# Performance work log

Measured on AMD Instinct MI355X. Metric: run time of the kernel, lower is better.

Reference implementation:

```python
import jax, jax.numpy as jnp
import numpy as np

N_NODES = 50000
N_GRAPHS = 128


def gcn_conv(x, edge_index, W, b, n_nodes):
    # PyG GCNConv: h = D^{-1/2}(A+I)D^{-1/2} (x W) + b
    h = x @ W  # [N, H]
    loop = jnp.arange(n_nodes)
    src = jnp.concatenate([edge_index[0], loop])
    dst = jnp.concatenate([edge_index[1], loop])
    deg = jax.ops.segment_sum(jnp.ones_like(dst, h.dtype), dst, num_segments=n_nodes)
    dinv = jnp.where(deg > 0, deg ** -0.5, 0.0)
    norm = dinv[src] * dinv[dst]  # [E+N]
    msgs = h[src] * norm[:, None]  # gather + normalize
    out = jax.ops.segment_sum(msgs, dst, num_segments=n_nodes)  # scatter-add
    return out + b


def setup_inputs() -> dict:
    key = jax.random.key(0)
    ks = jax.random.split(key, 8)
    F_in, H, L = 128, 128, 7
    x = jax.random.normal(ks[0], (N_NODES, F_in), dtype=jnp.float32)
    edge_index = jax.random.randint(ks[1], (2, 800000), 0, N_NODES, dtype=jnp.int64)
    batch = jnp.sort(jax.random.randint(ks[2], (N_NODES,), 0, N_GRAPHS, dtype=jnp.int64))
    s = lambda f: (1.0 / np.sqrt(f)).astype(np.float32)
    W1 = jax.random.normal(ks[3], (F_in, H), dtype=jnp.float32) * s(F_in)
    b1 = jnp.zeros((H,), jnp.float32)
    W2 = jax.random.normal(ks[4], (H, H), dtype=jnp.float32) * s(H)
    b2 = jnp.zeros((H,), jnp.float32)
    Wfc = jax.random.normal(ks[5], (H, L), dtype=jnp.float32) * s(H)
    bfc = jnp.zeros((L,), jnp.float32)
    return {"x": x, "edge_index": edge_index, "batch": batch,
            "W1": W1, "b1": b1, "W2": W2, "b2": b2, "Wfc": Wfc, "bfc": bfc}


def reference(x, edge_index, batch, W1, b1, W2, b2, Wfc, bfc):
    n = x.shape[0]
    h = jax.nn.relu(gcn_conv(x, edge_index, W1, b1, n))
    h = jax.nn.relu(gcn_conv(h, edge_index, W2, b2, n))
    # global_mean_pool over batch vector
    sums = jax.ops.segment_sum(h, batch, num_segments=N_GRAPHS)  # [G, H]
    cnt = jax.ops.segment_sum(jnp.ones((n,), h.dtype), batch, num_segments=N_GRAPHS)
    pooled = sums / jnp.maximum(cnt, 1.0)[:, None]
    return pooled @ Wfc + bfc  # [G, label_dim]
```

## Files before the change

kernel.cpp:

```cpp
#include <hip/hip_runtime.h>
#include <hip/hip_bf16.h>

#define HD 128
#define NL 7
#define BCAP 6144

typedef __attribute__((ext_vector_type(8))) short bf16x8;
typedef __attribute__((ext_vector_type(4))) float f32x4;

__device__ __forceinline__ unsigned short f2bf(float f) {
    __hip_bfloat16 b = __float2bfloat16(f);
    return *reinterpret_cast<unsigned short*>(&b);
}
__device__ __forceinline__ float bf2f(unsigned short u) {
    unsigned int x = ((unsigned int)u) << 16;
    return __uint_as_float(x);
}


__global__ __launch_bounds__(256) void k_prep(int* __restrict__ gbcur, int nb,
                                              float* __restrict__ sums, int m,
                                              const float* __restrict__ W1,
                                              const float* __restrict__ W2,
                                              unsigned short* __restrict__ Wt1,
                                              unsigned short* __restrict__ Wt2) {
    int i = blockIdx.x * 256 + threadIdx.x;
    if (i < nb) gbcur[i] = 0;
    if (i < m) sums[i] = 0.f;
    if (i < HD * HD) {
        int k = i >> 7, nn = i & 127;
        Wt1[nn * HD + k] = f2bf(W1[i]);
        Wt2[nn * HD + k] = f2bf(W2[i]);
    }
}


__global__ __launch_bounds__(256) void k_bucket(const int* __restrict__ src,
                                                const int* __restrict__ dst, int E,
                                                int* __restrict__ gbcur,
                                                int* __restrict__ stage, int nb) {
    __shared__ int lh[256];
    __shared__ int gb[256];
    int t = threadIdx.x;
    if (t < nb) lh[t] = 0;
    __syncthreads();

    int e0 = blockIdx.x * 4096;
    int bk[16]; int lr[16]; int rec[16];
    #pragma unroll
    for (int j = 0; j < 16; ++j) {
        int e = e0 + j * 256 + t;
        if (e < E) {
            int d = dst[e];
            int s = src[e];
            bk[j]  = d >> 8;
            rec[j] = ((d & 255) << 16) | s;
            lr[j]  = atomicAdd(&lh[bk[j]], 1);
        } else {
            bk[j] = -1; lr[j] = 0; rec[j] = 0;
        }
    }
    __syncthreads();
    if (t < nb) gb[t] = atomicAdd(&gbcur[t], lh[t]);
    __syncthreads();
    #pragma unroll
    for (int j = 0; j < 16; ++j) {
        if (bk[j] >= 0) {
            int p = gb[bk[j]] + lr[j];
            if (p < BCAP) stage[bk[j] * BCAP + p] = rec[j];
        }
    }
}


__global__ __launch_bounds__(256) void k_build_gemm1(
        const int* __restrict__ stage, const int* __restrict__ gbcnt,
        int* __restrict__ col, int* __restrict__ row_start,
        float* __restrict__ dinv,
        const float* __restrict__ X, const unsigned short* __restrict__ Wt,
        unsigned short* __restrict__ Y, int n, int nb) {
    __shared__ int rec_s[BCAP];
    __shared__ unsigned short rank_s[BCAP];
    __shared__ int hist[256];
    __shared__ int scan_s[256];
    __shared__ int base_s;
    int t = threadIdx.x;

    if ((int)blockIdx.x < nb) {
        int b = blockIdx.x;

        int cval = (t < nb) ? gbcnt[t] : 0;
        scan_s[t] = cval;
        __syncthreads();
        #pragma unroll
        for (int off = 1; off < 256; off <<= 1) {
            int v = (t >= off) ? scan_s[t - off] : 0;
            __syncthreads();
            scan_s[t] += v;
            __syncthreads();
        }
        if (t == b) base_s = scan_s[t] - cval;
        if (b == 0 && t == 0) row_start[n] = scan_s[nb - 1];
        __syncthreads();
        int base = base_s;
        int cnt  = min(gbcnt[b], BCAP);
        int node0 = b << 8;

        hist[t] = 0;
        __syncthreads();
        for (int e = t; e < cnt; e += 256) {
            int r = stage[b * BCAP + e];
            rec_s[e] = r;
            rank_s[e] = (unsigned short)atomicAdd(&hist[r >> 16], 1);
        }
        __syncthreads();

        int deg = hist[t];
        int node = node0 + t;
        if (node < n) dinv[node] = 1.0f / sqrtf((float)(deg + 1));

        scan_s[t] = deg;
        __syncthreads();
        #pragma unroll
        for (int off = 1; off < 256; off <<= 1) {
            int v = (t >= off) ? scan_s[t - off] : 0;
            __syncthreads();
            scan_s[t] += v;
            __syncthreads();
        }
        int lrs = scan_s[t] - deg;
        hist[t] = lrs;
        if (node < n) row_start[node] = base + lrs;
        __syncthreads();

        for (int e = t; e < cnt; e += 256) {
            int r = rec_s[e];
            col[base + hist[r >> 16] + rank_s[e]] = r & 0xFFFF;
        }
    } else {
        int wave = t >> 6, lane = t & 63;
        int lm = lane & 15, g = lane >> 4;
        int m0 = ((int)blockIdx.x - nb) * 64 + wave * 16;
        int row = m0 + lm;
        bool rok = row < n;

        f32x4 acc[8] = {};

        #pragma unroll
        for (int kb = 0; kb < 4; ++kb) {
            int k0 = kb * 32 + g * 8;
            bf16x8 a = {0, 0, 0, 0, 0, 0, 0, 0};
            if (rok) {
                const float* xp = X + (size_t)row * HD + k0;
                float4 v0 = *(const float4*)xp;
                float4 v1 = *(const float4*)(xp + 4);
                a[0] = (short)f2bf(v0.x); a[1] = (short)f2bf(v0.y);
                a[2] = (short)f2bf(v0.z); a[3] = (short)f2bf(v0.w);
                a[4] = (short)f2bf(v1.x); a[5] = (short)f2bf(v1.y);
                a[6] = (short)f2bf(v1.z); a[7] = (short)f2bf(v1.w);
            }
            #pragma unroll
            for (int nt = 0; nt < 8; ++nt) {
                int ncol = nt * 16 + lm;
                bf16x8 bfrag = *(const bf16x8*)(Wt + (size_t)ncol * HD + k0);
                acc[nt] = __builtin_amdgcn_mfma_f32_16x16x32_bf16(a, bfrag, acc[nt], 0, 0, 0);
            }
        }

        #pragma unroll
        for (int nt = 0; nt < 8; ++nt) {
            #pragma unroll
            for (int r = 0; r < 4; ++r) {
                int orow = m0 + g * 4 + r;
                if (orow < n) Y[(size_t)orow * HD + nt * 16 + lm] = f2bf(acc[nt][r]);
            }
        }
    }
}


__global__ __launch_bounds__(256) void k_gemm_mfma_bf(const unsigned short* __restrict__ X,
                                                      const unsigned short* __restrict__ Wt,
                                                      unsigned short* __restrict__ Y, int n) {
    int wave = threadIdx.x >> 6, lane = threadIdx.x & 63;
    int lm = lane & 15, g = lane >> 4;
    int m0 = blockIdx.x * 64 + wave * 16;
    int row = m0 + lm;
    bool rok = row < n;

    f32x4 acc[8] = {};

    #pragma unroll
    for (int kb = 0; kb < 4; ++kb) {
        int k0 = kb * 32 + g * 8;
        bf16x8 a = {0, 0, 0, 0, 0, 0, 0, 0};
        if (rok) a = *(const bf16x8*)(X + (size_t)row * HD + k0);
        #pragma unroll
        for (int nt = 0; nt < 8; ++nt) {
            int ncol = nt * 16 + lm;
            bf16x8 bfrag = *(const bf16x8*)(Wt + (size_t)ncol * HD + k0);
            acc[nt] = __builtin_amdgcn_mfma_f32_16x16x32_bf16(a, bfrag, acc[nt], 0, 0, 0);
        }
    }

    #pragma unroll
    for (int nt = 0; nt < 8; ++nt) {
        #pragma unroll
        for (int r = 0; r < 4; ++r) {
            int orow = m0 + g * 4 + r;
            if (orow < n) Y[(size_t)orow * HD + nt * 16 + lm] = f2bf(acc[nt][r]);
        }
    }
}


__global__ __launch_bounds__(256) void k_agg(const unsigned short* __restrict__ hin,
                                             const float* __restrict__ dinv,
                                             const int* __restrict__ row_start,
                                             const int* __restrict__ col,
                                             const float* __restrict__ bias,
                                             unsigned short* __restrict__ hout, int n) {
    int wave = threadIdx.x >> 6;
    int lane = threadIdx.x & 63;
    int v = blockIdx.x * 4 + wave;
    if (v >= n) return;

    int h  = lane >> 5;
    int li = lane & 31;
    int f  = li * 4;

    float dv = dinv[v];
    float a0 = 0.f, a1 = 0.f, a2 = 0.f, a3 = 0.f;

    int e  = row_start[v];
    int e1 = row_start[v + 1];

    for (; e + 8 <= e1; e += 8) {
        int s0 = col[e + h];
        int s1 = col[e + h + 2];
        int s2 = col[e + h + 4];
        int s3 = col[e + h + 6];
        float w0 = dinv[s0] * dv, w1 = dinv[s1] * dv;
        float w2 = dinv[s2] * dv, w3 = dinv[s3] * dv;
        ushort4 r0 = *(const ushort4*)(hin + (size_t)s0 * HD + f);
        ushort4 r1 = *(const ushort4*)(hin + (size_t)s1 * HD + f);
        ushort4 r2 = *(const ushort4*)(hin + (size_t)s2 * HD + f);
        ushort4 r3 = *(const ushort4*)(hin + (size_t)s3 * HD + f);
        a0 = fmaf(bf2f(r0.x), w0, a0); a1 = fmaf(bf2f(r0.y), w0, a1);
        a2 = fmaf(bf2f(r0.z), w0, a2); a3 = fmaf(bf2f(r0.w), w0, a3);
        a0 = fmaf(bf2f(r1.x), w1, a0); a1 = fmaf(bf2f(r1.y), w1, a1);
        a2 = fmaf(bf2f(r1.z), w1, a2); a3 = fmaf(bf2f(r1.w), w1, a3);
        a0 = fmaf(bf2f(r2.x), w2, a0); a1 = fmaf(bf2f(r2.y), w2, a1);
        a2 = fmaf(bf2f(r2.z), w2, a2); a3 = fmaf(bf2f(r2.w), w2, a3);
        a0 = fmaf(bf2f(r3.x), w3, a0); a1 = fmaf(bf2f(r3.y), w3, a1);
        a2 = fmaf(bf2f(r3.z), w3, a2); a3 = fmaf(bf2f(r3.w), w3, a3);
    }

    {
        #pragma unroll
        for (int j = 0; j < 4; ++j) {
            int idx = e + h + 2 * j;
            if (idx < e1) {
                int s = col[idx];
                float w = dinv[s] * dv;
                ushort4 r = *(const ushort4*)(hin + (size_t)s * HD + f);
                a0 = fmaf(bf2f(r.x), w, a0); a1 = fmaf(bf2f(r.y), w, a1);
                a2 = fmaf(bf2f(r.z), w, a2); a3 = fmaf(bf2f(r.w), w, a3);
            }
        }
    }

    a0 += __shfl_xor(a0, 32);
    a1 += __shfl_xor(a1, 32);
    a2 += __shfl_xor(a2, 32);
    a3 += __shfl_xor(a3, 32);

    if (h == 0) {
        ushort4 sv = *(const ushort4*)(hin + (size_t)v * HD + f);
        float selfw = dv * dv;
        float4 b = *(const float4*)(bias + f);
        ushort4 o;
        o.x = f2bf(fmaxf(fmaf(bf2f(sv.x), selfw, a0) + b.x, 0.f));
        o.y = f2bf(fmaxf(fmaf(bf2f(sv.y), selfw, a1) + b.y, 0.f));
        o.z = f2bf(fmaxf(fmaf(bf2f(sv.z), selfw, a2) + b.z, 0.f));
        o.w = f2bf(fmaxf(fmaf(bf2f(sv.w), selfw, a3) + b.w, 0.f));
        __builtin_nontemporal_store(*(unsigned long long*)&o,
            (unsigned long long*)(hout + (size_t)v * HD + f));
    }
}


__global__ __launch_bounds__(256) void k_agg_pool(const unsigned short* __restrict__ hin,
                                                  const float* __restrict__ dinv,
                                                  const int* __restrict__ row_start,
                                                  const int* __restrict__ col,
                                                  const float* __restrict__ bias,
                                                  const int* __restrict__ batch,
                                                  float* __restrict__ sums, int n) {
    __shared__ float lsum[4][HD];
    __shared__ int used[4];
    __shared__ int gbase_s;
    int t = threadIdx.x;

    if (t < 4) used[t] = 0;
    for (int i = t; i < 4 * HD; i += 256) ((float*)lsum)[i] = 0.f;
    int blk0 = blockIdx.x * 32;
    if (t == 0) gbase_s = batch[min(blk0, n - 1)];
    __syncthreads();
    int gbase = gbase_s;

    int wave = t >> 6;
    int lane = t & 63;
    int h  = lane >> 5;
    int li = lane & 31;
    int f  = li * 4;

    int v0 = blk0 + wave * 8;
    int vend = min(v0 + 8, n);

    float4 b = *(const float4*)(bias + f);
    float p0 = 0.f, p1 = 0.f, p2 = 0.f, p3 = 0.f;
    int curg = (v0 < n) ? batch[v0] : -1;

    for (int v = v0; v < vend; ++v) {
        float dv = dinv[v];
        float a0 = 0.f, a1 = 0.f, a2 = 0.f, a3 = 0.f;

        int e  = row_start[v];
        int e1 = row_start[v + 1];

        for (; e + 8 <= e1; e += 8) {
            int s0 = col[e + h];
            int s1 = col[e + h + 2];
            int s2 = col[e + h + 4];
            int s3 = col[e + h + 6];
            float w0 = dinv[s0] * dv, w1 = dinv[s1] * dv;
            float w2 = dinv[s2] * dv, w3 = dinv[s3] * dv;
            ushort4 r0 = *(const ushort4*)(hin + (size_t)s0 * HD + f);
            ushort4 r1 = *(const ushort4*)(hin + (size_t)s1 * HD + f);
            ushort4 r2 = *(const ushort4*)(hin + (size_t)s2 * HD + f);
            ushort4 r3 = *(const ushort4*)(hin + (size_t)s3 * HD + f);
            a0 = fmaf(bf2f(r0.x), w0, a0); a1 = fmaf(bf2f(r0.y), w0, a1);
            a2 = fmaf(bf2f(r0.z), w0, a2); a3 = fmaf(bf2f(r0.w), w0, a3);
            a0 = fmaf(bf2f(r1.x), w1, a0); a1 = fmaf(bf2f(r1.y), w1, a1);
            a2 = fmaf(bf2f(r1.z), w1, a2); a3 = fmaf(bf2f(r1.w), w1, a3);
            a0 = fmaf(bf2f(r2.x), w2, a0); a1 = fmaf(bf2f(r2.y), w2, a1);
            a2 = fmaf(bf2f(r2.z), w2, a2); a3 = fmaf(bf2f(r2.w), w2, a3);
            a0 = fmaf(bf2f(r3.x), w3, a0); a1 = fmaf(bf2f(r3.y), w3, a1);
            a2 = fmaf(bf2f(r3.z), w3, a2); a3 = fmaf(bf2f(r3.w), w3, a3);
        }

        #pragma unroll
        for (int j = 0; j < 4; ++j) {
            int idx = e + h + 2 * j;
            if (idx < e1) {
                int s = col[idx];
                float w = dinv[s] * dv;
                ushort4 r = *(const ushort4*)(hin + (size_t)s * HD + f);
                a0 = fmaf(bf2f(r.x), w, a0); a1 = fmaf(bf2f(r.y), w, a1);
                a2 = fmaf(bf2f(r.z), w, a2); a3 = fmaf(bf2f(r.w), w, a3);
            }
        }

        a0 += __shfl_xor(a0, 32);
        a1 += __shfl_xor(a1, 32);
        a2 += __shfl_xor(a2, 32);
        a3 += __shfl_xor(a3, 32);

        if (h == 0) {
            ushort4 sv = *(const ushort4*)(hin + (size_t)v * HD + f);
            float selfw = dv * dv;
            float ox = fmaxf(fmaf(bf2f(sv.x), selfw, a0) + b.x, 0.f);
            float oy = fmaxf(fmaf(bf2f(sv.y), selfw, a1) + b.y, 0.f);
            float oz = fmaxf(fmaf(bf2f(sv.z), selfw, a2) + b.z, 0.f);
            float ow = fmaxf(fmaf(bf2f(sv.w), selfw, a3) + b.w, 0.f);
            int g = batch[v];
            if (g != curg) {
                int slot = curg - gbase;
                if (slot >= 0 && slot < 4) {
                    atomicAdd(&lsum[slot][f],     p0);
                    atomicAdd(&lsum[slot][f + 1], p1);
                    atomicAdd(&lsum[slot][f + 2], p2);
                    atomicAdd(&lsum[slot][f + 3], p3);
                    used[slot] = 1;
                } else {
                    float* sp = sums + (size_t)curg * HD + f;
                    atomicAdd(sp,     p0);
                    atomicAdd(sp + 1, p1);
                    atomicAdd(sp + 2, p2);
                    atomicAdd(sp + 3, p3);
                }
                p0 = p1 = p2 = p3 = 0.f;
                curg = g;
            }
            p0 += ox; p1 += oy; p2 += oz; p3 += ow;
        }
    }

    if (h == 0 && curg >= 0) {
        int slot = curg - gbase;
        if (slot >= 0 && slot < 4) {
            atomicAdd(&lsum[slot][f],     p0);
            atomicAdd(&lsum[slot][f + 1], p1);
            atomicAdd(&lsum[slot][f + 2], p2);
            atomicAdd(&lsum[slot][f + 3], p3);
            used[slot] = 1;
        } else {
            float* sp = sums + (size_t)curg * HD + f;
            atomicAdd(sp,     p0);
            atomicAdd(sp + 1, p1);
            atomicAdd(sp + 2, p2);
            atomicAdd(sp + 3, p3);
        }
    }
    __syncthreads();

    int ff = t & 127;
    for (int s = t >> 7; s < 4; s += 2) {
        if (used[s]) {
            atomicAdd(&sums[(size_t)(gbase + s) * HD + ff], lsum[s][ff]);
        }
    }
}


__global__ __launch_bounds__(128) void k_fc(const float* __restrict__ sums,
                                            const int* __restrict__ batch,
                                            const float* __restrict__ Wfc,
                                            const float* __restrict__ bfc,
                                            float* __restrict__ out, int n) {
    int g = blockIdx.x;
    int t = threadIdx.x;
    __shared__ int slo, shi;
    if (t == 0) {
        int lo = 0, hi = n;
        while (lo < hi) { int m = (lo + hi) >> 1; if (batch[m] < g) lo = m + 1; else hi = m; }
        slo = lo;
        lo = 0; hi = n;
        while (lo < hi) { int m = (lo + hi) >> 1; if (batch[m] < g + 1) lo = m + 1; else hi = m; }
        shi = lo;
    }
    __syncthreads();
    float cnt = (float)(shi - slo);
    __shared__ float sp[HD];
    sp[t] = sums[(size_t)g * HD + t] / fmaxf(cnt, 1.f);
    __syncthreads();
    if (t < NL) {
        float o = bfc[t];
        for (int k = 0; k < HD; ++k) o = fmaf(sp[k], Wfc[k * NL + t], o);
        out[g * NL + t] = o;
    }
}


extern "C" void kernel_launch(void* const* d_in, const int* in_sizes, int n_in,
                              void* d_out, int out_size, void* d_ws, size_t ws_size,
                              hipStream_t stream) {
    const float* x    = (const float*)d_in[0];
    const int*   ei   = (const int*)d_in[1];
    const int*   batch= (const int*)d_in[2];
    const float* W1   = (const float*)d_in[3];
    const float* b1   = (const float*)d_in[4];
    const float* W2   = (const float*)d_in[5];
    const float* b2   = (const float*)d_in[6];
    const float* Wfc  = (const float*)d_in[7];
    const float* bfc  = (const float*)d_in[8];
    float* out = (float*)d_out;

    int n = in_sizes[0] / HD;
    int E = in_sizes[1] / 2;
    int G = out_size / NL;
    const int* srcp = ei;
    const int* dstp = ei + E;

    int nb = (n + 255) >> 8;

    char* ws = (char*)d_ws;
    auto align256 = [](size_t v) { return (v + 255) & ~(size_t)255; };
    size_t o = 0;
    int*   row_start = (int*)(ws + o); o = align256(o + (size_t)(n + 1) * 4);
    int*   gbcur     = (int*)(ws + o); o = align256(o + (size_t)nb * 4);
    float* dinv      = (float*)(ws + o); o = align256(o + (size_t)n * 4);
    int*   col       = (int*)(ws + o); o = align256(o + (size_t)E * 4);
    unsigned short* tmp  = (unsigned short*)(ws + o); o = align256(o + (size_t)n * HD * 2);
    unsigned short* tmp2 = (unsigned short*)(ws + o); o = align256(o + (size_t)n * HD * 2);
    int*   stage     = (int*)(ws + o); o = align256(o + (size_t)nb * BCAP * 4);
    float* sums      = (float*)(ws + o); o = align256(o + (size_t)G * HD * 4);
    unsigned short* Wt1 = (unsigned short*)(ws + o); o = align256(o + (size_t)HD * HD * 2);
    unsigned short* Wt2 = (unsigned short*)(ws + o); o = align256(o + (size_t)HD * HD * 2);

    int mZero = G * HD;
    k_prep<<<(HD * HD + 255) / 256, 256, 0, stream>>>(gbcur, nb, sums, mZero,
                                                      W1, W2, Wt1, Wt2);

    int nblkC = (E + 4095) / 4096;
    k_bucket<<<nblkC, 256, 0, stream>>>(srcp, dstp, E, gbcur, stage, nb);

    int gemmBlocks = (n + 63) / 64;
    k_build_gemm1<<<nb + gemmBlocks, 256, 0, stream>>>(stage, gbcur, col, row_start,
                                                       dinv, x, Wt1, tmp, n, nb);

    k_agg<<<(n + 3) / 4, 256, 0, stream>>>(tmp, dinv, row_start, col, b1, tmp2, n);
    k_gemm_mfma_bf<<<gemmBlocks, 256, 0, stream>>>(tmp2, Wt2, tmp, n);
    k_agg_pool<<<(n + 31) / 32, 256, 0, stream>>>(tmp, dinv, row_start, col, b2,
                                                  batch, sums, n);

    k_fc<<<G, 128, 0, stream>>>(sums, batch, Wfc, bfc, out, n);
}
```

Baseline: 161.2 us.

## Store first GEMM output in feature-sliced layout and aggregate per slice

```diff
diff --git a/kernel.cpp b/kernel.cpp
--- a/kernel.cpp
+++ b/kernel.cpp
@@ -172,7 +172,8 @@
             #pragma unroll
             for (int r = 0; r < 4; ++r) {
                 int orow = m0 + g * 4 + r;
-                if (orow < n) Y[(size_t)orow * HD + nt * 16 + lm] = f2bf(acc[nt][r]);
+                if (orow < n)
+                    Y[((size_t)nt * n + orow) * 16 + lm] = f2bf(acc[nt][r]);
             }
         }
     }
@@ -214,78 +215,71 @@
 }
 
 
-__global__ __launch_bounds__(256) void k_agg(const unsigned short* __restrict__ hin,
-                                             const float* __restrict__ dinv,
-                                             const int* __restrict__ row_start,
-                                             const int* __restrict__ col,
-                                             const float* __restrict__ bias,
-                                             unsigned short* __restrict__ hout, int n) {
+__global__ __launch_bounds__(256) void k_agg_slice(
+        const unsigned short* __restrict__ hin_s,
+        const float* __restrict__ dinv,
+        const int* __restrict__ row_start,
+        const int* __restrict__ col,
+        const float* __restrict__ bias,
+        unsigned short* __restrict__ hout, int n) {
+    int slice = blockIdx.x & 7;
+    int nblk  = blockIdx.x >> 3;
     int wave = threadIdx.x >> 6;
     int lane = threadIdx.x & 63;
-    int v = blockIdx.x * 4 + wave;
+    int v = nblk * 4 + wave;
     if (v >= n) return;
 
-    int h  = lane >> 5;
-    int li = lane & 31;
-    int f  = li * 4;
+    int ge = lane >> 3;
+    int lg = lane & 7;
+    int fis = lg * 2;
+
+    const unsigned short* hsl = hin_s + (size_t)slice * n * 16;
 
     float dv = dinv[v];
-    float a0 = 0.f, a1 = 0.f, a2 = 0.f, a3 = 0.f;
-
-    int e  = row_start[v];
-    int e1 = row_start[v + 1];
-
-    for (; e + 8 <= e1; e += 8) {
-        int s0 = col[e + h];
-        int s1 = col[e + h + 2];
-        int s2 = col[e + h + 4];
-        int s3 = col[e + h + 6];
-        float w0 = dinv[s0] * dv, w1 = dinv[s1] * dv;
-        float w2 = dinv[s2] * dv, w3 = dinv[s3] * dv;
-        ushort4 r0 = *(const ushort4*)(hin + (size_t)s0 * HD + f);
-        ushort4 r1 = *(const ushort4*)(hin + (size_t)s1 * HD + f);
-        ushort4 r2 = *(const ushort4*)(hin + (size_t)s2 * HD + f);
-        ushort4 r3 = *(const ushort4*)(hin + (size_t)s3 * HD + f);
-        a0 = fmaf(bf2f(r0.x), w0, a0); a1 = fmaf(bf2f(r0.y), w0, a1);
-        a2 = fmaf(bf2f(r0.z), w0, a2); a3 = fmaf(bf2f(r0.w), w0, a3);
-        a0 = fmaf(bf2f(r1.x), w1, a0); a1 = fmaf(bf2f(r1.y), w1, a1);
-        a2 = fmaf(bf2f(r1.z), w1, a2); a3 = fmaf(bf2f(r1.w), w1, a3);
-        a0 = fmaf(bf2f(r2.x), w2, a0); a1 = fmaf(bf2f(r2.y), w2, a1);
-        a2 = fmaf(bf2f(r2.z), w2, a2); a3 = fmaf(bf2f(r2.w), w2, a3);
-        a0 = fmaf(bf2f(r3.x), w3, a0); a1 = fmaf(bf2f(r3.y), w3, a1);
-        a2 = fmaf(bf2f(r3.z), w3, a2); a3 = fmaf(bf2f(r3.w), w3, a3);
-    }
-
+    float accx = 0.f, accy = 0.f;
+
+    int e = row_start[v], e1 = row_start[v + 1];
+
+    for (; e + 16 <= e1; e += 16) {
+        int s0 = col[e + ge];
+        int s1 = col[e + ge + 8];
+        float w0 = dinv[s0] * dv;
+        float w1 = dinv[s1] * dv;
+        ushort2 r0 = *(const ushort2*)(hsl + (size_t)s0 * 16 + fis);
+        ushort2 r1 = *(const ushort2*)(hsl + (size_t)s1 * 16 + fis);
+        accx = fmaf(bf2f(r0.x), w0, accx); accy = fmaf(bf2f(r0.y), w0, accy);
+        accx = fmaf(bf2f(r1.x), w1, accx); accy = fmaf(bf2f(r1.y), w1, accy);
+    }
+    if (e + 8 <= e1) {
+        int s = col[e + ge];
+        float w = dinv[s] * dv;
+        ushort2 r = *(const ushort2*)(hsl + (size_t)s * 16 + fis);
+        accx = fmaf(bf2f(r.x), w, accx); accy = fmaf(bf2f(r.y), w, accy);
+        e += 8;
+    }
     {
-        #pragma unroll
-        for (int j = 0; j < 4; ++j) {
-            int idx = e + h + 2 * j;
-            if (idx < e1) {
-                int s = col[idx];
-                float w = dinv[s] * dv;
-                ushort4 r = *(const ushort4*)(hin + (size_t)s * HD + f);
-                a0 = fmaf(bf2f(r.x), w, a0); a1 = fmaf(bf2f(r.y), w, a1);
-                a2 = fmaf(bf2f(r.z), w, a2); a3 = fmaf(bf2f(r.w), w, a3);
-            }
-        }
-    }
-
-    a0 += __shfl_xor(a0, 32);
-    a1 += __shfl_xor(a1, 32);
-    a2 += __shfl_xor(a2, 32);
-    a3 += __shfl_xor(a3, 32);
-
-    if (h == 0) {
-        ushort4 sv = *(const ushort4*)(hin + (size_t)v * HD + f);
+        int idx = e + ge;
+        if (idx < e1) {
+            int s = col[idx];
+            float w = dinv[s] * dv;
+            ushort2 r = *(const ushort2*)(hsl + (size_t)s * 16 + fis);
+            accx = fmaf(bf2f(r.x), w, accx); accy = fmaf(bf2f(r.y), w, accy);
+        }
+    }
+
+    accx += __shfl_xor(accx, 8);  accy += __shfl_xor(accy, 8);
+    accx += __shfl_xor(accx, 16); accy += __shfl_xor(accy, 16);
+    accx += __shfl_xor(accx, 32); accy += __shfl_xor(accy, 32);
+
+    if (ge == 0) {
+        ushort2 sv = *(const ushort2*)(hsl + (size_t)v * 16 + fis);
         float selfw = dv * dv;
-        float4 b = *(const float4*)(bias + f);
-        ushort4 o;
-        o.x = f2bf(fmaxf(fmaf(bf2f(sv.x), selfw, a0) + b.x, 0.f));
-        o.y = f2bf(fmaxf(fmaf(bf2f(sv.y), selfw, a1) + b.y, 0.f));
-        o.z = f2bf(fmaxf(fmaf(bf2f(sv.z), selfw, a2) + b.z, 0.f));
-        o.w = f2bf(fmaxf(fmaf(bf2f(sv.w), selfw, a3) + b.w, 0.f));
-        __builtin_nontemporal_store(*(unsigned long long*)&o,
-            (unsigned long long*)(hout + (size_t)v * HD + f));
+        int fg = slice * 16 + fis;
+        float2 b = *(const float2*)(bias + fg);
+        ushort2 o;
+        o.x = f2bf(fmaxf(fmaf(bf2f(sv.x), selfw, accx) + b.x, 0.f));
+        o.y = f2bf(fmaxf(fmaf(bf2f(sv.y), selfw, accy) + b.y, 0.f));
+        *(ushort2*)(hout + (size_t)v * HD + fg) = o;
     }
 }
 
@@ -500,7 +494,8 @@
     k_build_gemm1<<<nb + gemmBlocks, 256, 0, stream>>>(stage, gbcur, col, row_start,
                                                        dinv, x, Wt1, tmp, n, nb);
 
-    k_agg<<<(n + 3) / 4, 256, 0, stream>>>(tmp, dinv, row_start, col, b1, tmp2, n);
+    k_agg_slice<<<8 * ((n + 3) / 4), 256, 0, stream>>>(tmp, dinv, row_start, col,
+                                                       b1, tmp2, n);
     k_gemm_mfma_bf<<<gemmBlocks, 256, 0, stream>>>(tmp2, Wt2, tmp, n);
     k_agg_pool<<<(n + 31) / 32, 256, 0, stream>>>(tmp, dinv, row_start, col, b2,
                                                   batch, sums, n);
```

Measured after the change: 226.2 us. 40.3% more time.

## Fuse layer-1 aggregation with layer-2 GEMM via shared-memory row tile

Applied to the files above, without the earlier changes.

```diff
diff --git a/kernel.cpp b/kernel.cpp
--- a/kernel.cpp
+++ b/kernel.cpp
@@ -179,113 +179,113 @@
 }
 
 
-__global__ __launch_bounds__(256) void k_gemm_mfma_bf(const unsigned short* __restrict__ X,
-                                                      const unsigned short* __restrict__ Wt,
-                                                      unsigned short* __restrict__ Y, int n) {
-    int wave = threadIdx.x >> 6, lane = threadIdx.x & 63;
+__global__ __launch_bounds__(256) void k_agg_gemm2(
+        const unsigned short* __restrict__ hin,
+        const float* __restrict__ dinv,
+        const int* __restrict__ row_start,
+        const int* __restrict__ col,
+        const float* __restrict__ bias,
+        const unsigned short* __restrict__ Wt2,
+        unsigned short* __restrict__ Y,
+        int n) {
+    __shared__ __attribute__((aligned(16))) unsigned short arow[16][136];
+    int t = threadIdx.x;
+    int wave = t >> 6;
+    int lane = t & 63;
+    int h  = lane >> 5;
+    int li = lane & 31;
+    int f  = li * 4;
+    int node0 = blockIdx.x * 16;
+
+    float4 b = *(const float4*)(bias + f);
+
+    #pragma unroll 1
+    for (int i = 0; i < 4; ++i) {
+        int vloc = wave * 4 + i;
+        int v = node0 + vloc;
+        if (v < n) {
+            float dv = dinv[v];
+            float a0 = 0.f, a1 = 0.f, a2 = 0.f, a3 = 0.f;
+
+            int e  = row_start[v];
+            int e1 = row_start[v + 1];
+
+            for (; e + 8 <= e1; e += 8) {
+                int s0 = col[e + h];
+                int s1 = col[e + h + 2];
+                int s2 = col[e + h + 4];
+                int s3 = col[e + h + 6];
+                float w0 = dinv[s0] * dv, w1 = dinv[s1] * dv;
+                float w2 = dinv[s2] * dv, w3 = dinv[s3] * dv;
+                ushort4 r0 = *(const ushort4*)(hin + (size_t)s0 * HD + f);
+                ushort4 r1 = *(const ushort4*)(hin + (size_t)s1 * HD + f);
+                ushort4 r2 = *(const ushort4*)(hin + (size_t)s2 * HD + f);
+                ushort4 r3 = *(const ushort4*)(hin + (size_t)s3 * HD + f);
+                a0 = fmaf(bf2f(r0.x), w0, a0); a1 = fmaf(bf2f(r0.y), w0, a1);
+                a2 = fmaf(bf2f(r0.z), w0, a2); a3 = fmaf(bf2f(r0.w), w0, a3);
+                a0 = fmaf(bf2f(r1.x), w1, a0); a1 = fmaf(bf2f(r1.y), w1, a1);
+                a2 = fmaf(bf2f(r1.z), w1, a2); a3 = fmaf(bf2f(r1.w), w1, a3);
+                a0 = fmaf(bf2f(r2.x), w2, a0); a1 = fmaf(bf2f(r2.y), w2, a1);
+                a2 = fmaf(bf2f(r2.z), w2, a2); a3 = fmaf(bf2f(r2.w), w2, a3);
+                a0 = fmaf(bf2f(r3.x), w3, a0); a1 = fmaf(bf2f(r3.y), w3, a1);
+                a2 = fmaf(bf2f(r3.z), w3, a2); a3 = fmaf(bf2f(r3.w), w3, a3);
+            }
+
+            #pragma unroll
+            for (int j = 0; j < 4; ++j) {
+                int idx = e + h + 2 * j;
+                if (idx < e1) {
+                    int s = col[idx];
+                    float w = dinv[s] * dv;
+                    ushort4 r = *(const ushort4*)(hin + (size_t)s * HD + f);
+                    a0 = fmaf(bf2f(r.x), w, a0); a1 = fmaf(bf2f(r.y), w, a1);
+                    a2 = fmaf(bf2f(r.z), w, a2); a3 = fmaf(bf2f(r.w), w, a3);
+                }
+            }
+
+            a0 += __shfl_xor(a0, 32);
+            a1 += __shfl_xor(a1, 32);
+            a2 += __shfl_xor(a2, 32);
+            a3 += __shfl_xor(a3, 32);
+
+            if (h == 0) {
+                ushort4 sv = *(const ushort4*)(hin + (size_t)v * HD + f);
+                float selfw = dv * dv;
+                ushort4 o;
+                o.x = f2bf(fmaxf(fmaf(bf2f(sv.x), selfw, a0) + b.x, 0.f));
+                o.y = f2bf(fmaxf(fmaf(bf2f(sv.y), selfw, a1) + b.y, 0.f));
+                o.z = f2bf(fmaxf(fmaf(bf2f(sv.z), selfw, a2) + b.z, 0.f));
+                o.w = f2bf(fmaxf(fmaf(bf2f(sv.w), selfw, a3) + b.w, 0.f));
+                *(ushort4*)&arow[vloc][f] = o;
+            }
+        } else if (h == 0) {
+            ushort4 z; z.x = z.y = z.z = z.w = 0;
+            *(ushort4*)&arow[vloc][f] = z;
+        }
+    }
+    __syncthreads();
+
     int lm = lane & 15, g = lane >> 4;
-    int m0 = blockIdx.x * 64 + wave * 16;
-    int row = m0 + lm;
-    bool rok = row < n;
-
-    f32x4 acc[8] = {};
-
+    f32x4 acc[2] = {};
     #pragma unroll
     for (int kb = 0; kb < 4; ++kb) {
         int k0 = kb * 32 + g * 8;
-        bf16x8 a = {0, 0, 0, 0, 0, 0, 0, 0};
-        if (rok) a = *(const bf16x8*)(X + (size_t)row * HD + k0);
-        #pragma unroll
-        for (int nt = 0; nt < 8; ++nt) {
-            int ncol = nt * 16 + lm;
-            bf16x8 bfrag = *(const bf16x8*)(Wt + (size_t)ncol * HD + k0);
-            acc[nt] = __builtin_amdgcn_mfma_f32_16x16x32_bf16(a, bfrag, acc[nt], 0, 0, 0);
-        }
-    }
-
+        bf16x8 a = *(const bf16x8*)&arow[lm][k0];
+        #pragma unroll
+        for (int j = 0; j < 2; ++j) {
+            int ncol = (wave * 2 + j) * 16 + lm;
+            bf16x8 bfrag = *(const bf16x8*)(Wt2 + (size_t)ncol * HD + k0);
+            acc[j] = __builtin_amdgcn_mfma_f32_16x16x32_bf16(a, bfrag, acc[j], 0, 0, 0);
+        }
+    }
     #pragma unroll
-    for (int nt = 0; nt < 8; ++nt) {
+    for (int j = 0; j < 2; ++j) {
+        int nc0 = (wave * 2 + j) * 16;
         #pragma unroll
         for (int r = 0; r < 4; ++r) {
-            int orow = m0 + g * 4 + r;
-            if (orow < n) Y[(size_t)orow * HD + nt * 16 + lm] = f2bf(acc[nt][r]);
-        }
-    }
-}
-
-
-__global__ __launch_bounds__(256) void k_agg(const unsigned short* __restrict__ hin,
-                                             const float* __restrict__ dinv,
-                                             const int* __restrict__ row_start,
-                                             const int* __restrict__ col,
-                                             const float* __restrict__ bias,
-                                             unsigned short* __restrict__ hout, int n) {
-    int wave = threadIdx.x >> 6;
-    int lane = threadIdx.x & 63;
-    int v = blockIdx.x * 4 + wave;
-    if (v >= n) return;
-
-    int h  = lane >> 5;
-    int li = lane & 31;
-    int f  = li * 4;
-
-    float dv = dinv[v];
-    float a0 = 0.f, a1 = 0.f, a2 = 0.f, a3 = 0.f;
-
-    int e  = row_start[v];
-    int e1 = row_start[v + 1];
-
-    for (; e + 8 <= e1; e += 8) {
-        int s0 = col[e + h];
-        int s1 = col[e + h + 2];
-        int s2 = col[e + h + 4];
-        int s3 = col[e + h + 6];
-        float w0 = dinv[s0] * dv, w1 = dinv[s1] * dv;
-        float w2 = dinv[s2] * dv, w3 = dinv[s3] * dv;
-        ushort4 r0 = *(const ushort4*)(hin + (size_t)s0 * HD + f);
-        ushort4 r1 = *(const ushort4*)(hin + (size_t)s1 * HD + f);
-        ushort4 r2 = *(const ushort4*)(hin + (size_t)s2 * HD + f);
-        ushort4 r3 = *(const ushort4*)(hin + (size_t)s3 * HD + f);
-        a0 = fmaf(bf2f(r0.x), w0, a0); a1 = fmaf(bf2f(r0.y), w0, a1);
-        a2 = fmaf(bf2f(r0.z), w0, a2); a3 = fmaf(bf2f(r0.w), w0, a3);
-        a0 = fmaf(bf2f(r1.x), w1, a0); a1 = fmaf(bf2f(r1.y), w1, a1);
-        a2 = fmaf(bf2f(r1.z), w1, a2); a3 = fmaf(bf2f(r1.w), w1, a3);
-        a0 = fmaf(bf2f(r2.x), w2, a0); a1 = fmaf(bf2f(r2.y), w2, a1);
-        a2 = fmaf(bf2f(r2.z), w2, a2); a3 = fmaf(bf2f(r2.w), w2, a3);
-        a0 = fmaf(bf2f(r3.x), w3, a0); a1 = fmaf(bf2f(r3.y), w3, a1);
-        a2 = fmaf(bf2f(r3.z), w3, a2); a3 = fmaf(bf2f(r3.w), w3, a3);
-    }
-
-    {
-        #pragma unroll
-        for (int j = 0; j < 4; ++j) {
-            int idx = e + h + 2 * j;
-            if (idx < e1) {
-                int s = col[idx];
-                float w = dinv[s] * dv;
-                ushort4 r = *(const ushort4*)(hin + (size_t)s * HD + f);
-                a0 = fmaf(bf2f(r.x), w, a0); a1 = fmaf(bf2f(r.y), w, a1);
-                a2 = fmaf(bf2f(r.z), w, a2); a3 = fmaf(bf2f(r.w), w, a3);
-            }
-        }
-    }
-
-    a0 += __shfl_xor(a0, 32);
-    a1 += __shfl_xor(a1, 32);
-    a2 += __shfl_xor(a2, 32);
-    a3 += __shfl_xor(a3, 32);
-
-    if (h == 0) {
-        ushort4 sv = *(const ushort4*)(hin + (size_t)v * HD + f);
-        float selfw = dv * dv;
-        float4 b = *(const float4*)(bias + f);
-        ushort4 o;
-        o.x = f2bf(fmaxf(fmaf(bf2f(sv.x), selfw, a0) + b.x, 0.f));
-        o.y = f2bf(fmaxf(fmaf(bf2f(sv.y), selfw, a1) + b.y, 0.f));
-        o.z = f2bf(fmaxf(fmaf(bf2f(sv.z), selfw, a2) + b.z, 0.f));
-        o.w = f2bf(fmaxf(fmaf(bf2f(sv.w), selfw, a3) + b.w, 0.f));
-        __builtin_nontemporal_store(*(unsigned long long*)&o,
-            (unsigned long long*)(hout + (size_t)v * HD + f));
+            int v = node0 + g * 4 + r;
+            if (v < n) Y[(size_t)v * HD + nc0 + lm] = f2bf(acc[j][r]);
+        }
     }
 }
 
@@ -500,9 +500,9 @@
     k_build_gemm1<<<nb + gemmBlocks, 256, 0, stream>>>(stage, gbcur, col, row_start,
                                                        dinv, x, Wt1, tmp, n, nb);
 
-    k_agg<<<(n + 3) / 4, 256, 0, stream>>>(tmp, dinv, row_start, col, b1, tmp2, n);
-    k_gemm_mfma_bf<<<gemmBlocks, 256, 0, stream>>>(tmp2, Wt2, tmp, n);
-    k_agg_pool<<<(n + 31) / 32, 256, 0, stream>>>(tmp, dinv, row_start, col, b2,
+    k_agg_gemm2<<<(n + 15) / 16, 256, 0, stream>>>(tmp, dinv, row_start, col,
+                                                   b1, Wt2, tmp2, n);
+    k_agg_pool<<<(n + 31) / 32, 256, 0, stream>>>(tmp2, dinv, row_start, col, b2,
                                                   batch, sums, n);
 
     k_fc<<<G, 128, 0, stream>>>(sums, batch, Wfc, bfc, out, n);
```

After: 150.6 us, median of 2. 1.07x faster.
